# Kernel optimization log

Hardware: AMD Instinct MI355X
Metric: run time of the kernel (lower is better)

## Reference

```python
import jax, jax.numpy as jnp
import numpy as np

EPS = 1e-5
INTER = 10
EXTRACT_SEQ = 400 // INTER  # 40


def _layernorm(x, gamma=None, beta=None):
    # LayerNorm over last axis, eps=1e-5 (torch default)
    mu = jnp.mean(x, axis=-1, keepdims=True)
    var = jnp.var(x, axis=-1, keepdims=True)
    y = (x - mu) * jax.lax.rsqrt(var + EPS)
    if gamma is not None:
        y = y * gamma + beta
    return y


def setup_inputs() -> dict:
    key = jax.random.key(0)
    ks = jax.random.split(key, 4)
    b, o, c, s = 64, 16, 128, 400
    x = jax.random.normal(ks[0], (b, o, c, s), dtype=jnp.float32)
    scale = 1.0 / np.sqrt(c)
    Wq = jax.random.normal(ks[1], (c, c), dtype=jnp.float32) * scale
    Wk = jax.random.normal(ks[2], (c, c), dtype=jnp.float32) * scale
    Wp = jax.random.normal(ks[3], (c, c), dtype=jnp.float32) * scale
    z = jnp.zeros((c,), dtype=jnp.float32)
    one = jnp.ones((c,), dtype=jnp.float32)
    return {
        "x": x,
        "Wq": Wq, "bq": z, "gq": one, "betaq": z,
        "Wk": Wk, "bk": z, "gk": one, "betak": z,
        "Wp": Wp, "bp": z, "gp": one, "betap": z,
    }


def reference(x, Wq, bq, gq, betaq, Wk, bk, gk, betak, Wp, bp, gp, betap):
    # x: [b, o, c, s]
    temp = jnp.swapaxes(x, -1, -2)                 # [b,o,s,c]
    temp = _layernorm(temp)                        # fresh LN, unit affine

    # query/key: Linear + LN (dropout = identity in eval)
    q = _layernorm(temp @ Wq.T + bq, gq, betaq)    # [b,o,s,c]
    k = _layernorm(temp @ Wk.T + bk, gk, betak)    # [b,o,s,c]
    q = jnp.swapaxes(q, -1, -2)                    # [b,o,c,s]
    k = jnp.swapaxes(k, -1, -2)

    # AvgPool over s with kernel=stride=inter
    b_, o_, c_, s_ = q.shape
    qp = q.reshape(b_, o_, c_, s_ // INTER, INTER).mean(-1)  # [b,o,c,40]
    kp = k.reshape(b_, o_, c_, s_ // INTER, INTER).mean(-1)

    scaling = EXTRACT_SEQ ** 0.5
    atten = jnp.einsum('bocs,boms->bocm', qp, kp) / scaling  # [b,o,c,c]
    score = jax.nn.softmax(atten, axis=-1)

    # einsum 'b o c s, b o c m -> b o c s': sums score over m only
    out = x * jnp.sum(score, axis=-1, keepdims=True)         # [b,o,c,s]

    out = jnp.swapaxes(out, -1, -2)                           # [b,o,s,c]
    out = _layernorm(out @ Wp.T + bp, gp, betap)
    out = jnp.swapaxes(out, -1, -2)                           # [b,o,c,s]
    return out + x
```

## Files before the change

### kernel.cpp

```cpp
#include <hip/hip_runtime.h>
#include <hip/hip_bf16.h>


#define BO 1024
#define CC 128
#define SS 400
#define TS 80
#define NW 5
#define NT (NW * 64)
#define XSTRIDE 82

typedef __attribute__((ext_vector_type(8))) short short8;
typedef __attribute__((ext_vector_type(4))) float f32x4;

__global__ void wp_cvt_kernel(const float* __restrict__ wp,
                              __hip_bfloat16* __restrict__ out) {
    int i = blockIdx.x * 256 + threadIdx.x;
    out[i] = __float2bfloat16(wp[i]);
}

__global__ __launch_bounds__(NT) void ca_main_kernel(
    const float* __restrict__ x,
    const __hip_bfloat16* __restrict__ wpb,
    const float* __restrict__ bp,
    const float* __restrict__ gp,
    const float* __restrict__ betap,
    float* __restrict__ out)
{
    __shared__ float xs[CC * XSTRIDE];

    const int bo = blockIdx.y;
    const int s0 = blockIdx.x * TS;
    const int t  = threadIdx.x;
    const size_t base = (size_t)bo * (CC * SS);

    {
        const int r   = t / 20;
        const int col = (t % 20) * 4;
        #pragma unroll
        for (int it = 0; it < 8; ++it) {
            const int c = it * 16 + r;
            const float4 v = *reinterpret_cast<const float4*>(
                x + base + (size_t)c * SS + s0 + col);
            const int di = c * XSTRIDE + col;
            *reinterpret_cast<float2*>(&xs[di])     = make_float2(v.x, v.y);
            *reinterpret_cast<float2*>(&xs[di + 2]) = make_float2(v.z, v.w);
        }
    }
    __syncthreads();

    const int lane = t & 63;
    const int wid  = t >> 6;
    const int lcol = lane & 15;
    const int lgrp = lane >> 4;
    const int scol = wid * 16 + lcol;

    short8 bfrag[4];
    #pragma unroll
    for (int kk = 0; kk < 4; ++kk) {
        #pragma unroll
        for (int i = 0; i < 8; ++i) {
            const int k = kk * 32 + lgrp * 8 + i;
            const float f = xs[k * XSTRIDE + scol];
            const __hip_bfloat16 h = __float2bfloat16(f);
            bfrag[kk][i] = (short)__builtin_bit_cast(unsigned short, h);
        }
    }

    f32x4 acc[8];
    #pragma unroll
    for (int m = 0; m < 8; ++m) acc[m] = (f32x4){0.f, 0.f, 0.f, 0.f};

    const short8* wpa = reinterpret_cast<const short8*>(wpb);
    #pragma unroll
    for (int kk = 0; kk < 4; ++kk) {
        #pragma unroll
        for (int m = 0; m < 8; ++m) {
            const short8 a = wpa[((m * 16 + lcol) * CC + kk * 32 + lgrp * 8) >> 3];
            acc[m] = __builtin_amdgcn_mfma_f32_16x16x32_bf16(a, bfrag[kk], acc[m], 0, 0, 0);
        }
    }

    float sum = 0.f, sq = 0.f;
    #pragma unroll
    for (int m = 0; m < 8; ++m) {
        #pragma unroll
        for (int j = 0; j < 4; ++j) {
            const int c = m * 16 + lgrp * 4 + j;
            const float z = acc[m][j] + bp[c];
            acc[m][j] = z;
            sum += z;
            sq  += z * z;
        }
    }
    sum += __shfl_xor(sum, 16);
    sum += __shfl_xor(sum, 32);
    sq  += __shfl_xor(sq, 16);
    sq  += __shfl_xor(sq, 32);

    const float mean = sum * (1.f / 128.f);
    const float var  = sq * (1.f / 128.f) - mean * mean;
    const float rinv = rsqrtf(var + 1e-5f);

    float* op = out + base + s0 + scol;
    #pragma unroll
    for (int m = 0; m < 8; ++m) {
        #pragma unroll
        for (int j = 0; j < 4; ++j) {
            const int c = m * 16 + lgrp * 4 + j;
            const float y = (acc[m][j] - mean) * rinv * gp[c] + betap[c]
                          + xs[c * XSTRIDE + scol];
            op[(size_t)c * SS] = y;
        }
    }
}

extern "C" void kernel_launch(void* const* d_in, const int* in_sizes, int n_in,
                              void* d_out, int out_size, void* d_ws, size_t ws_size,
                              hipStream_t stream) {
    const float* x     = (const float*)d_in[0];
    const float* Wp    = (const float*)d_in[9];
    const float* bp    = (const float*)d_in[10];
    const float* gp    = (const float*)d_in[11];
    const float* betap = (const float*)d_in[12];
    __hip_bfloat16* wpb = (__hip_bfloat16*)d_ws;

    wp_cvt_kernel<<<dim3(64), dim3(256), 0, stream>>>(Wp, wpb);
    ca_main_kernel<<<dim3(SS / TS, BO), dim3(NT), 0, stream>>>(
        x, wpb, bp, gp, betap, (float*)d_out);
}
```

Before: 443.5 us.

## Stage Wp in swizzled LDS via direct loads; read x straight to registers

The x tile is no longer staged through shared memory. Each lane loads its column of x directly from global memory into registers for the B fragments and re-reads x from global for the residual add. Wp is instead pre-swizzled during the bf16 conversion and copied into LDS with global_load_lds, so the MFMA A operands come from LDS with an XOR swizzle rather than from global/L1. A launch bound of 5 blocks per CU is added. The risk is uncoalesced strided x loads (a column per lane) and a second global read of x for the residual.

New measurement: 414.6 us. -6.5%, faster.

```diff
diff --git a/kernel.cpp b/kernel.cpp
--- a/kernel.cpp
+++ b/kernel.cpp
@@ -2,88 +2,89 @@
 #include <hip/hip_bf16.h>
 
 
-#define BO 1024
 #define CC 128
 #define SS 400
-#define TS 80
-#define NW 5
-#define NT (NW * 64)
-#define XSTRIDE 82
+#define NT 320
 
 typedef __attribute__((ext_vector_type(8))) short short8;
 typedef __attribute__((ext_vector_type(4))) float f32x4;
 
 __global__ void wp_cvt_kernel(const float* __restrict__ wp,
-                              __hip_bfloat16* __restrict__ out) {
-    int i = blockIdx.x * 256 + threadIdx.x;
-    out[i] = __float2bfloat16(wp[i]);
+                              unsigned short* __restrict__ wpb) {
+    const int e = blockIdx.x * 256 + threadIdx.x;
+    const int L = e << 1;
+    const int B = L ^ (((L >> 8) & 7) << 4);
+    const __hip_bfloat16 h = __float2bfloat16(wp[B >> 1]);
+    wpb[e] = __builtin_bit_cast(unsigned short, h);
 }
 
-__global__ __launch_bounds__(NT) void ca_main_kernel(
+__global__ __launch_bounds__(NT, 5) void ca_main_kernel(
     const float* __restrict__ x,
-    const __hip_bfloat16* __restrict__ wpb,
+    const unsigned short* __restrict__ wpb,
     const float* __restrict__ bp,
     const float* __restrict__ gp,
     const float* __restrict__ betap,
     float* __restrict__ out)
 {
-    __shared__ float xs[CC * XSTRIDE];
+    __shared__ unsigned short As[CC * CC];
 
-    const int bo = blockIdx.y;
-    const int s0 = blockIdx.x * TS;
-    const int t  = threadIdx.x;
-    const size_t base = (size_t)bo * (CC * SS);
-
-    {
-        const int r   = t / 20;
-        const int col = (t % 20) * 4;
-        #pragma unroll
-        for (int it = 0; it < 8; ++it) {
-            const int c = it * 16 + r;
-            const float4 v = *reinterpret_cast<const float4*>(
-                x + base + (size_t)c * SS + s0 + col);
-            const int di = c * XSTRIDE + col;
-            *reinterpret_cast<float2*>(&xs[di])     = make_float2(v.x, v.y);
-            *reinterpret_cast<float2*>(&xs[di + 2]) = make_float2(v.z, v.w);
-        }
-    }
-    __syncthreads();
-
+    const int bo   = blockIdx.y;
+    const int s0   = blockIdx.x * 80;
+    const int t    = threadIdx.x;
     const int lane = t & 63;
     const int wid  = t >> 6;
     const int lcol = lane & 15;
     const int lgrp = lane >> 4;
-    const int scol = wid * 16 + lcol;
+    const int scol = s0 + wid * 16 + lcol;
+    const size_t base = (size_t)bo * (CC * SS);
+    const float* xb = x + base + scol;
+
+    float raw[32];
+    #pragma unroll
+    for (int kk = 0; kk < 4; ++kk)
+        #pragma unroll
+        for (int i = 0; i < 8; ++i)
+            raw[kk * 8 + i] = xb[(size_t)(kk * 32 + lgrp * 8 + i) * SS];
+
+    for (int j = wid; j < 32; j += 5) {
+        __builtin_amdgcn_global_load_lds(
+            (const __attribute__((address_space(1))) unsigned int*)
+                ((const char*)wpb + j * 1024 + lane * 16),
+            (__attribute__((address_space(3))) unsigned int*)
+                ((char*)As + j * 1024),
+            16, 0, 0);
+    }
 
     short8 bfrag[4];
     #pragma unroll
-    for (int kk = 0; kk < 4; ++kk) {
+    for (int kk = 0; kk < 4; ++kk)
         #pragma unroll
         for (int i = 0; i < 8; ++i) {
-            const int k = kk * 32 + lgrp * 8 + i;
-            const float f = xs[k * XSTRIDE + scol];
-            const __hip_bfloat16 h = __float2bfloat16(f);
+            const __hip_bfloat16 h = __float2bfloat16(raw[kk * 8 + i]);
             bfrag[kk][i] = (short)__builtin_bit_cast(unsigned short, h);
         }
-    }
+
+    __syncthreads();
 
     f32x4 acc[8];
     #pragma unroll
     for (int m = 0; m < 8; ++m) acc[m] = (f32x4){0.f, 0.f, 0.f, 0.f};
 
-    const short8* wpa = reinterpret_cast<const short8*>(wpb);
+    const int axor = (lcol & 7) << 4;
+    const char* asb = (const char*)As;
     #pragma unroll
     for (int kk = 0; kk < 4; ++kk) {
         #pragma unroll
         for (int m = 0; m < 8; ++m) {
-            const short8 a = wpa[((m * 16 + lcol) * CC + kk * 32 + lgrp * 8) >> 3];
+            const short8 a = *reinterpret_cast<const short8*>(
+                asb + ((((m * 16 + lcol) * 256) + kk * 64 + lgrp * 16) ^ axor));
             acc[m] = __builtin_amdgcn_mfma_f32_16x16x32_bf16(a, bfrag[kk], acc[m], 0, 0, 0);
         }
     }
 
     float sum = 0.f, sq = 0.f;
     #pragma unroll
-    for (int m = 0; m < 8; ++m) {
+    for (int m = 0; m < 8; ++m)
         #pragma unroll
         for (int j = 0; j < 4; ++j) {
             const int c = m * 16 + lgrp * 4 + j;
@@ -92,7 +93,6 @@
             sum += z;
             sq  += z * z;
         }
-    }
     sum += __shfl_xor(sum, 16);
     sum += __shfl_xor(sum, 32);
     sq  += __shfl_xor(sq, 16);
@@ -102,17 +102,16 @@
     const float var  = sq * (1.f / 128.f) - mean * mean;
     const float rinv = rsqrtf(var + 1e-5f);
 
-    float* op = out + base + s0 + scol;
+    float* op = out + base + scol;
     #pragma unroll
-    for (int m = 0; m < 8; ++m) {
+    for (int m = 0; m < 8; ++m)
         #pragma unroll
         for (int j = 0; j < 4; ++j) {
             const int c = m * 16 + lgrp * 4 + j;
             const float y = (acc[m][j] - mean) * rinv * gp[c] + betap[c]
-                          + xs[c * XSTRIDE + scol];
+                          + xb[(size_t)c * SS];
             op[(size_t)c * SS] = y;
         }
-    }
 }
 
 extern "C" void kernel_launch(void* const* d_in, const int* in_sizes, int n_in,
@@ -123,9 +122,9 @@
     const float* bp    = (const float*)d_in[10];
     const float* gp    = (const float*)d_in[11];
     const float* betap = (const float*)d_in[12];
-    __hip_bfloat16* wpb = (__hip_bfloat16*)d_ws;
+    unsigned short* wpb = (unsigned short*)d_ws;
 
     wp_cvt_kernel<<<dim3(64), dim3(256), 0, stream>>>(Wp, wpb);
-    ca_main_kernel<<<dim3(SS / TS, BO), dim3(NT), 0, stream>>>(
+    ca_main_kernel<<<dim3(SS / 80, 1024), dim3(NT), 0, stream>>>(
         x, wpb, bp, gp, betap, (float*)d_out);
 }
```
